# Performance work log

Measured on AMD Instinct MI355X. Metric: run time of the kernel, lower is better.

## Reference

```python
import jax, jax.numpy as jnp
import numpy as np

B, S, D, H = 4, 1024, 1024, 16
DH = D // H
NEG = -10000.0  # mask fill value for non-float32 (bool) masks in the torch code


def setup_inputs() -> dict:
    key = jax.random.key(0)
    ks = jax.random.split(key, 16)
    scale = 0.02
    inp = {
        "query": jax.random.normal(ks[0], (B, S, D), jnp.float32),
        "key": jax.random.normal(ks[1], (B, S, D), jnp.float32),
        "value": jax.random.normal(ks[2], (B, S, D), jnp.float32),
        "pos_embedding": jax.random.normal(ks[3], (B, S, D), jnp.float32),
        # learned params (torch Linear convention: y = x @ W.T + b, W is (out,in))
        "Wq": jax.random.normal(ks[4], (D, D), jnp.float32) * scale,
        "bq": jnp.zeros((D,), jnp.float32),
        "Wk": jax.random.normal(ks[5], (D, D), jnp.float32) * scale,
        "bk": jnp.zeros((D,), jnp.float32),
        "Wv": jax.random.normal(ks[6], (D, D), jnp.float32) * scale,
        "bv": jnp.zeros((D,), jnp.float32),
        "Wpos": jax.random.normal(ks[7], (D, D), jnp.float32) * scale,
        "u_bias": jax.random.normal(ks[8], (H, DH), jnp.float32) * scale,
        "v_bias": jax.random.normal(ks[9], (H, DH), jnp.float32) * scale,
        "Wout": jax.random.normal(ks[10], (D, D), jnp.float32) * scale,
        "bout": jnp.zeros((D,), jnp.float32),
    }
    # right-padding mask: lengths in [S//2, S]; mask[b,i,j] = pad(i) | pad(j)
    lengths = jax.random.randint(ks[11], (B,), S // 2, S + 1)
    pad = jnp.arange(S)[None, :] >= lengths[:, None]  # (B,S)
    inp["mask"] = pad[:, :, None] | pad[:, None, :]  # (B,S,S) bool
    return inp


def _relative_shift(pos_score, mask):
    """Batch-safe Transformer-XL relative shift (vectorized version of the
    per-batch python loop). pos_score: (B,H,S,S), mask: (B,S,S) bool."""
    b, h, s, _ = pos_score.shape
    # per-row true length: S - number of padded rows (column 0 is never padded)
    L = s - jnp.sum(mask[:, :, 0].astype(jnp.int32), axis=-1)  # (B,)
    i = jnp.arange(s)[:, None]
    j = jnp.arange(s)[None, :]

    def shift_one(ps, Lb):  # ps: (H,S,S), Lb: scalar int
        # padded[h,r,0]=0; padded[h,r,k]=ps[h,r,k-1]; flat index of out[i,j] in
        # the (Lb+1, Lb) reshape of padded[:, :Lb, :Lb+1], rows 1: -> offset Lb
        m = Lb + i * Lb + j            # (S,S)
        row = m // (Lb + 1)
        col = m % (Lb + 1)
        g = ps[:, jnp.clip(row, 0, s - 1), jnp.clip(col - 1, 0, s - 1)]  # (H,S,S)
        valid = (i < Lb) & (j < Lb) & (col != 0)
        return jnp.where(valid[None], g, jnp.zeros((), ps.dtype))

    shifted = jax.vmap(shift_one)(pos_score, L)
    # masked_fill_(padding_mask, 0.0)
    return jnp.where(mask[:, None, :, :], jnp.zeros((), pos_score.dtype), shifted)


def reference(query, key, value, pos_embedding, mask,
              Wq, bq, Wk, bk, Wv, bv, Wpos, u_bias, v_bias, Wout, bout):
    b = query.shape[0]
    sqrt_dim = np.sqrt(D).astype(np.float32)

    q = (query @ Wq.T + bq).reshape(b, -1, H, DH)                 # (B,S,H,dh)
    k = (key @ Wk.T + bk).reshape(b, -1, H, DH)                   # (B,S,H,dh)
    v = (value @ Wv.T + bv).reshape(b, -1, H, DH)                 # (B,S,H,dh)
    p = (pos_embedding @ Wpos.T).reshape(b, -1, H, DH)            # (B,S,H,dh)

    content_score = jnp.einsum('bqhd,bkhd->bhqk', q + u_bias, k)  # (B,H,S,S)
    pos_score = jnp.einsum('bqhd,bkhd->bhqk', q + v_bias, p)      # (B,H,S,S)
    pos_score = _relative_shift(pos_score, mask)

    score = (content_score + pos_score) / sqrt_dim
    m4 = mask[:, None, :, :]
    score = jnp.where(m4, NEG, score)
    attn = jax.nn.softmax(score, axis=-1)
    attn = jnp.where(m4, jnp.zeros((), attn.dtype), attn)
    # dropout is identity in eval mode
    context = jnp.einsum('bhqk,bkhd->bqhd', attn, v).reshape(b, -1, D)
    return context @ Wout.T + bout
```

## Files before the change

### kernel.cpp

```cpp
#include <hip/hip_runtime.h>

#define B_ 4
#define S_ 1024
#define D_ 1024
#define H_ 16
#define DH_ 64
#define OOS 0.03125f

#define QPL (1088 * 64)
#define KPL (1024 * 64)
#define VPL (1024 * 64)
#define PPL (200 * 1024)
#define PADLO 1056

#define APL_SW (256 * 32 * 512)
#define WPL_SW (64 * 32 * 512)

typedef __attribute__((ext_vector_type(8))) short short8;
typedef __attribute__((ext_vector_type(4))) float f32x4;
typedef const __attribute__((address_space(1))) unsigned int* gas_t;
typedef __attribute__((address_space(3))) unsigned int* las_t;

__device__ __forceinline__ ushort f2bf(float x) {
  unsigned u = __float_as_uint(x);
  unsigned r = u + 0x7fffu + ((u >> 16) & 1u);
  return (ushort)(r >> 16);
}
__device__ __forceinline__ float bf2f(ushort u) {
  return __uint_as_float(((unsigned)u) << 16);
}

union pack8 { ushort u[8]; uint4 v; };

struct ConvDesc { const float* src; ushort* hi; ushort* lo; };
struct ConvArgs { ConvDesc d[5]; };

__global__ __launch_bounds__(256) void conv_split(ConvArgs args)
{
  const ConvDesc dd = args.d[blockIdx.y];
  const int tt = blockIdx.x;
  const int tid = threadIdx.x;
  const float* src = dd.src + (size_t)tt * 16 * 1024;
  ushort* hi = dd.hi + (size_t)tt * 32 * 512;
  ushort* lo = dd.lo + (size_t)tt * 32 * 512;
#pragma unroll 4
  for (int q = 0; q < 16; ++q) {
    const int s = q * 256 + tid;
    const int r = s >> 8, c4 = s & 255;
    const float4 x = *(const float4*)(src + r * 1024 + c4 * 4);
    const int k = c4 * 4;
    const size_t addr = (size_t)(k >> 5) * 512 + ((k & 31) >> 3) * 128 + r * 8 + (k & 7);
    ushort4 hu, lu;
    hu.x = f2bf(x.x); lu.x = f2bf(x.x - bf2f(hu.x));
    hu.y = f2bf(x.y); lu.y = f2bf(x.y - bf2f(hu.y));
    hu.z = f2bf(x.z); lu.z = f2bf(x.z - bf2f(hu.z));
    hu.w = f2bf(x.w); lu.w = f2bf(x.w - bf2f(hu.w));
    *(ushort4*)(hi + addr) = hu;
    *(ushort4*)(lo + addr) = lu;
  }
}

template <int MODE>
__global__ __launch_bounds__(256, 2) void gemm_bf16x3(
    const ushort* __restrict__ Ahi, const ushort* __restrict__ Alo,
    const ushort* __restrict__ Bhi, const ushort* __restrict__ Blo,
    const float* __restrict__ bias, float* __restrict__ C,
    ushort* __restrict__ O1, ushort* __restrict__ O2,
    const float* __restrict__ ub, const float* __restrict__ vb)
{
  __shared__ __align__(16) ushort SM[12288];
  const int tid = threadIdx.x;
  const int wave = tid >> 6, lane = tid & 63;
  const int m16 = lane & 15, quad = lane >> 4;
  const int mw2 = wave & 1, nw2 = wave >> 1;
  const int mt0 = blockIdx.y * 4;
  const int nt0 = blockIdx.x * 8;

  f32x4 acc[2][4];
#pragma unroll
  for (int mf = 0; mf < 2; ++mf)
#pragma unroll
    for (int nf = 0; nf < 4; ++nf) acc[mf][nf] = (f32x4){0.f, 0.f, 0.f, 0.f};

  for (int kb = 0; kb < 32; ++kb) {
    __syncthreads();
    for (int t = wave; t < 24; t += 4) {
      const ushort* g;
      int l;
      if (t < 4)       { g = Ahi + ((size_t)(mt0 + t) * 32 + kb) * 512;      l = t * 512; }
      else if (t < 8)  { g = Alo + ((size_t)(mt0 + t - 4) * 32 + kb) * 512;  l = 2048 + (t - 4) * 512; }
      else if (t < 16) { g = Bhi + ((size_t)(nt0 + t - 8) * 32 + kb) * 512;  l = 4096 + (t - 8) * 512; }
      else             { g = Blo + ((size_t)(nt0 + t - 16) * 32 + kb) * 512; l = 8192 + (t - 16) * 512; }
      __builtin_amdgcn_global_load_lds((gas_t)(g + lane * 8), (las_t)(SM + l), 16, 0, 0);
    }
    __syncthreads();
    short8 ah[2], al[2], bh[4], bl[4];
#pragma unroll
    for (int mf = 0; mf < 2; ++mf) {
      ah[mf] = *(const short8*)(SM + (mw2 * 2 + mf) * 512 + lane * 8);
      al[mf] = *(const short8*)(SM + 2048 + (mw2 * 2 + mf) * 512 + lane * 8);
    }
#pragma unroll
    for (int nf = 0; nf < 4; ++nf) {
      bh[nf] = *(const short8*)(SM + 4096 + (nw2 * 4 + nf) * 512 + lane * 8);
      bl[nf] = *(const short8*)(SM + 8192 + (nw2 * 4 + nf) * 512 + lane * 8);
    }
#pragma unroll
    for (int mf = 0; mf < 2; ++mf)
#pragma unroll
      for (int nf = 0; nf < 4; ++nf) {
        acc[mf][nf] = __builtin_amdgcn_mfma_f32_16x16x32_bf16(ah[mf], bh[nf], acc[mf][nf], 0, 0, 0);
        acc[mf][nf] = __builtin_amdgcn_mfma_f32_16x16x32_bf16(ah[mf], bl[nf], acc[mf][nf], 0, 0, 0);
        acc[mf][nf] = __builtin_amdgcn_mfma_f32_16x16x32_bf16(al[mf], bh[nf], acc[mf][nf], 0, 0, 0);
      }
  }

  const int Mb = blockIdx.y * 64, Nb = blockIdx.x * 128;
  float* const E = (float*)SM;
#pragma unroll
  for (int c = 0; c < 2; ++c) {
    __syncthreads();
    if (nw2 == c) {
#pragma unroll
      for (int mf = 0; mf < 2; ++mf)
#pragma unroll
        for (int nf = 0; nf < 4; ++nf)
#pragma unroll
          for (int reg = 0; reg < 4; ++reg)
            E[(mw2 * 32 + mf * 16 + quad * 4 + reg) * 64 + nf * 16 + m16] = acc[mf][nf][reg];
    }
    __syncthreads();

    if (MODE == 3) {
#pragma unroll
      for (int q = 0; q < 2; ++q) {
        const int s = tid + 256 * q;
        const int cc = s & 63, rg = s >> 6;
        const int tok0 = Mb + rg * 8;
        const int n = Nb + c * 64 + cc;
        const int bb = tok0 >> 10, jr = tok0 & 1023;
        const int jt = jr >> 6, ksj = (jr >> 5) & 1, qk = (jr >> 3) & 3;
        const int h = n >> 6, dd = n & 63;
        const int subd = dd >> 4, nn = dd & 15;
        const size_t base = (size_t)(bb * 16 + h) * VPL + (size_t)jt * 4096 +
                            (size_t)(subd * 2 + ksj) * 512 + (qk * 16 + nn) * 8;
        const float bvv = bias[n];
        pack8 p;
#pragma unroll
        for (int i = 0; i < 8; ++i) p.u[i] = f2bf(E[(rg * 8 + i) * 64 + cc] + bvv);
        *(uint4*)(O1 + base) = p.v;
      }
    } else {
#pragma unroll
      for (int q = 0; q < 2; ++q) {
        const int s = tid + 256 * q;
        const int r = s >> 3, g = s & 7;
        const int token = Mb + r;
        const int n = Nb + c * 64 + g * 8;
        float v[8];
        *(float4*)&v[0] = *(const float4*)&E[r * 64 + g * 8];
        *(float4*)&v[4] = *(const float4*)&E[r * 64 + g * 8 + 4];
        if (MODE == 0) {
          float4 o0, o1;
          o0.x = v[0] + bias[n + 0]; o0.y = v[1] + bias[n + 1];
          o0.z = v[2] + bias[n + 2]; o0.w = v[3] + bias[n + 3];
          o1.x = v[4] + bias[n + 4]; o1.y = v[5] + bias[n + 5];
          o1.z = v[6] + bias[n + 6]; o1.w = v[7] + bias[n + 7];
          *(float4*)(C + (size_t)token * 1024 + n) = o0;
          *(float4*)(C + (size_t)token * 1024 + n + 4) = o1;
        } else if (MODE == 1) {
          const int bb = token >> 10, sr = token & 1023;
          const int h = n >> 6, d = n & 63;
          const size_t base = (size_t)(bb * 16 + h) * QPL + (size_t)sr * 64 + d;
          pack8 pu, pv;
#pragma unroll
          for (int j = 0; j < 8; ++j) {
            const float qv_ = v[j] + bias[n + j];
            pu.u[j] = f2bf(qv_ + ub[n + j]);
            pv.u[j] = f2bf(qv_ + vb[n + j]);
          }
          *(uint4*)(O1 + base) = pu.v;
          *(uint4*)(O2 + base) = pv.v;
        } else {
          const int bb = token >> 10, jr = token & 1023;
          const int h = n >> 6, dd = n & 63;
          const int ks = dd >> 5, qk = (dd >> 3) & 3;
          size_t base;
          if (MODE == 2)
            base = (size_t)(bb * 16 + h) * KPL + (size_t)(jr >> 6) * 4096 +
                   (size_t)((((jr >> 4) & 3) * 2 + ks)) * 512 + (qk * 16 + (jr & 15)) * 8;
          else {
            const int ro = jr + PADLO;
            base = (size_t)(bb * 16 + h) * PPL + (size_t)(ro >> 4) * 1024 +
                   (size_t)ks * 512 + (qk * 16 + (ro & 15)) * 8;
          }
          pack8 p;
#pragma unroll
          for (int j = 0; j < 8; ++j)
            p.u[j] = f2bf(v[j] + (MODE == 2 ? bias[n + j] : 0.f));
          *(uint4*)(O1 + base) = p.v;
        }
      }
    }
  }
}

__global__ void len_kernel(const int* __restrict__ mask, int* __restrict__ len,
                           ushort* __restrict__ Psw)
{
  const int b = blockIdx.x;
  int cnt = 0;
  for (int i = threadIdx.x; i < S_; i += 256)
    cnt += (mask[(size_t)b * S_ * S_ + (size_t)i * S_] != 0) ? 1 : 0;
  __shared__ int sh[256];
  sh[threadIdx.x] = cnt;
  __syncthreads();
  for (int off = 128; off > 0; off >>= 1) {
    if (threadIdx.x < off) sh[threadIdx.x] += sh[threadIdx.x + off];
    __syncthreads();
  }
  if (threadIdx.x == 0) len[b] = S_ - sh[0];
  for (int idx = threadIdx.x; idx < 16 * 64; idx += 256) {
    const int h = idx >> 6, d = idx & 63;
    Psw[(size_t)(b * 16 + h) * PPL + 65 * 1024 + (d >> 5) * 512 +
        (((d >> 3) & 3) * 16 + 15) * 8 + (d & 7)] = 0;
  }
}

__global__ __launch_bounds__(512, 4) void attn_mfma2(
    const ushort* __restrict__ Qu, const ushort* __restrict__ Qv,
    const ushort* __restrict__ Ksw, const ushort* __restrict__ Vsw,
    const ushort* __restrict__ Psw, const int* __restrict__ len,
    float* __restrict__ CTX)
{
  __shared__ __align__(16) ushort SMEM[26624];
  __shared__ float mrow[64], lrow[64], arow[64];

  ushort* const Ks_  = SMEM;
  ushort* const Vts_ = SMEM + 4096;
  ushort* const P1s_ = SMEM + 8192;
  ushort* const P2s_ = SMEM + 17408;
  float*  const sc   = (float*)(SMEM + 8192);
  ushort* const Pb   = SMEM + 17408;

  const int tid  = threadIdx.x;
  const int wave = tid >> 6, lane = tid & 63;
  const int hw   = wave >> 2, w4 = wave & 3;
  const int m16  = lane & 15, quad = lane >> 4;
  const int mw   = w4 & 1,  nw   = w4 >> 1;
  const int koff0 = quad * 8;

  const int base = blockIdx.x * 64;
  const int i0 = base + hw * 32;
  const int h  = blockIdx.y;
  const int b  = blockIdx.z;
  const int ph = b * 16 + h;
  const int L  = len[b];
  const size_t gb = ((size_t)b * S_) * D_ + h * DH_;

  if (base >= L) {
    for (int idx = tid; idx < 64 * 64; idx += 512) {
      const int r = idx >> 6, d = idx & 63;
      CTX[gb + (size_t)(base + r) * D_ + d] = 0.f;
    }
    return;
  }
  const bool active = (i0 < L);

  const ushort* quP = Qu + (size_t)ph * QPL;
  const ushort* qvP = Qv + (size_t)ph * QPL;
  short8 qufr[2][2], qvfr[2][2][2];
#pragma unroll
  for (int Mt = 0; Mt < 2; ++Mt)
#pragma unroll
    for (int ks = 0; ks < 2; ++ks) {
      qufr[Mt][ks] = *(const short8*)(quP + (size_t)(i0 + 16 * Mt + m16) * 64 + ks * 32 + koff0);
#pragma unroll
      for (int off = 0; off < 2; ++off)
        qvfr[off][Mt][ks] =
            *(const short8*)(qvP + (size_t)(i0 + off + 16 * Mt + m16) * 64 + ks * 32 + koff0);
    }

  if (tid < 64) { mrow[tid] = -3.0e38f; lrow[tid] = 0.f; arow[tid] = 0.f; }

  f32x4 ctx0 = {0.f, 0.f, 0.f, 0.f}, ctx1 = {0.f, 0.f, 0.f, 0.f};

  const ushort* ksP = Ksw + (size_t)ph * KPL;
  const ushort* vsP = Vsw + (size_t)ph * VPL;
  const ushort* psP = Psw + (size_t)ph * PPL;

  for (int j0 = 0; j0 < L; j0 += 64) {
    __syncthreads();

    const int jt = j0 >> 6;
    const int A1 = L - 32 - i0 + j0, A2 = j0 - i0 - 33;
    const int ro1 = A1 + PADLO, ro2 = A2 + PADLO;
    const int rb1 = ro1 >> 4, rb2 = ro2 >> 4;
    const int d1 = ro1 & 15, d2 = ro2 & 15;
    const int rb1lo = (L - 64 - base + j0 + PADLO) >> 4;
    const int rb2lo = (j0 - base - 65 + PADLO) >> 4;
    const ushort* P1h = P1s_ + ((rb1 - rb1lo) << 10);
    const ushort* P2h = P2s_ + ((rb2 - rb2lo) << 10);

    {
      const ushort* kgo = ksP + (size_t)jt * 4096;
      const ushort* vgo = vsP + (size_t)jt * 4096;
      const ushort* p1o = psP + (size_t)rb1lo * 1024;
      const ushort* p2o = psP + (size_t)rb2lo * 1024;
      for (int t = wave; t < 52; t += 8) {
        const ushort* g;
        int l;
        if (t < 8)       { g = kgo + t * 512;        l = t * 512; }
        else if (t < 16) { g = vgo + (t - 8) * 512;  l = 4096 + (t - 8) * 512; }
        else if (t < 34) { g = p1o + (t - 16) * 512; l = 8192 + (t - 16) * 512; }
        else             { g = p2o + (t - 34) * 512; l = 17408 + (t - 34) * 512; }
        __builtin_amdgcn_global_load_lds((gas_t)(g + lane * 8), (las_t)(SMEM + l), 16, 0, 0);
      }
    }
    __syncthreads();

    const int jrem = L - j0;
    const int jmax = (jrem < 64) ? jrem : 64;
    const int cthr = 31 + i0 - j0;

    f32x4 av[9];
#pragma unroll
    for (int t = 0; t < 9; ++t) {
      const int id = w4 + 4 * t;
      f32x4 a = {0.f, 0.f, 0.f, 0.f};
      if (active) {
        if (id < 8) {
          const int Mt = id & 1, Nt = id >> 1;
          if (16 * Nt < jmax) {
            const ushort* bp = Ks_ + (Nt * 2) * 512 + lane * 8;
            a = __builtin_amdgcn_mfma_f32_16x16x32_bf16(qufr[Mt][0], *(const short8*)bp, a, 0, 0, 0);
            a = __builtin_amdgcn_mfma_f32_16x16x32_bf16(qufr[Mt][1], *(const short8*)(bp + 512), a, 0, 0, 0);
          }
        } else if (id < 22) {
          const int e = id - 8, Mt = e & 1, Ntp = e >> 1;
          const int sm = 16 * (Ntp + Mt);
          if (sm >= d1 + 1 && sm <= jmax + d1 + 30 && 16 * Ntp - d1 <= cthr) {
            const ushort* bp = P1h + (Ntp * 2) * 512 + lane * 8;
            a = __builtin_amdgcn_mfma_f32_16x16x32_bf16(qvfr[0][Mt][0], *(const short8*)bp, a, 0, 0, 0);
            a = __builtin_amdgcn_mfma_f32_16x16x32_bf16(qvfr[0][Mt][1], *(const short8*)(bp + 512), a, 0, 0, 0);
          }
        } else {
          const int e = id - 22, Mt = e & 1, Ntp = e >> 1;
          const int sm = 16 * (Ntp + Mt);
          if (sm >= d2 + 1 && sm <= jmax + d2 + 30 && 16 * Ntp + 15 - d2 > cthr) {
            const ushort* bp = P2h + (Ntp * 2) * 512 + lane * 8;
            a = __builtin_amdgcn_mfma_f32_16x16x32_bf16(qvfr[1][Mt][0], *(const short8*)bp, a, 0, 0, 0);
            a = __builtin_amdgcn_mfma_f32_16x16x32_bf16(qvfr[1][Mt][1], *(const short8*)(bp + 512), a, 0, 0, 0);
          }
        }
      }
      av[t] = a;
    }
    __syncthreads();

#pragma unroll
    for (int t = 0; t < 2; ++t) {
      const int id = w4 + 4 * t;
      if (id < 8) {
        const int Mt = id & 1, Nt = id >> 1;
        if (16 * Nt < jmax) {
#pragma unroll
          for (int reg = 0; reg < 4; ++reg)
            sc[(hw * 32 + 16 * Mt + quad * 4 + reg) * 68 + 16 * Nt + m16] =
                active ? av[t][reg] : 0.f;
        }
      }
    }
    __syncthreads();

    if (active) {
#pragma unroll
      for (int t = 0; t < 9; ++t) {
        const int id = w4 + 4 * t;
        if (id >= 8) {
          const bool isG2 = id >= 22;
          const int e = id - (isG2 ? 22 : 8), Mt = e & 1, Ntp = e >> 1;
          const int dl = isG2 ? d2 : d1;
          const int sm = 16 * (Ntp + Mt);
          const bool use = sm >= dl + 1 && sm <= jmax + dl + 30 &&
                           (isG2 ? (16 * Ntp + 15 - dl > cthr) : (16 * Ntp - dl <= cthr));
          if (use) {
            const int c = 16 * Ntp + m16 - dl;
            const bool sel = isG2 ? (c > cthr) : (c <= cthr);
            if (sel) {
#pragma unroll
              for (int reg = 0; reg < 4; ++reg) {
                const int il = 16 * Mt + quad * 4 + reg;
                const int jl = c - 31 + il;
                if (jl >= 0 && jl < 64) sc[(hw * 32 + il) * 68 + jl] += av[t][reg];
              }
            }
          }
        }
      }
    }
    __syncthreads();

    {
      const int row = tid >> 3, t8 = tid & 7, jb = t8 * 8;
      const float* sr = sc + row * 68 + jb;
      float mx = -3.0e38f;
#pragma unroll
      for (int q = 0; q < 8; ++q)
        if (jb + q < jmax) mx = fmaxf(mx, sr[q]);
#pragma unroll
      for (int off = 1; off < 8; off <<= 1)
        mx = fmaxf(mx, __shfl_xor(mx, off, 64));
      if (t8 == 0) {
        const float mo = mrow[row];
        const float mn = fmaxf(mo, mx);
        arow[row] = __expf((mo - mn) * OOS);
        mrow[row] = mn;
      }
    }
    __syncthreads();
    {
      const int row = tid >> 3, t8 = tid & 7, jb = t8 * 8;
      const float m = mrow[row];
      const float* sr = sc + row * 68 + jb;
      float e[8], s = 0.f;
#pragma unroll
      for (int q = 0; q < 8; ++q) {
        float v = 0.f;
        if (jb + q < jmax) v = __expf((sr[q] - m) * OOS);
        e[q] = v;
        s += v;
      }
      ushort4 u0, u1;
      u0.x = f2bf(e[0]); u0.y = f2bf(e[1]); u0.z = f2bf(e[2]); u0.w = f2bf(e[3]);
      u1.x = f2bf(e[4]); u1.y = f2bf(e[5]); u1.z = f2bf(e[6]); u1.w = f2bf(e[7]);
      *(ushort4*)&Pb[row * 72 + jb] = u0;
      *(ushort4*)&Pb[row * 72 + jb + 4] = u1;
#pragma unroll
      for (int off = 1; off < 8; off <<= 1) s += __shfl_xor(s, off, 64);
      if (t8 == 0) lrow[row] = lrow[row] * arow[row] + s;
    }
    __syncthreads();

    if (active) {
      float al[4];
#pragma unroll
      for (int reg = 0; reg < 4; ++reg) al[reg] = arow[hw * 32 + 16 * mw + quad * 4 + reg];
#pragma unroll
      for (int reg = 0; reg < 4; ++reg) { ctx0[reg] *= al[reg]; ctx1[reg] *= al[reg]; }
      const ushort* ap = Pb + (hw * 32 + 16 * mw + m16) * 72;
#pragma unroll
      for (int ksj = 0; ksj < 2; ++ksj) {
        const short8 a = *(const short8*)(ap + ksj * 32 + koff0);
        ctx0 = __builtin_amdgcn_mfma_f32_16x16x32_bf16(
            a, *(const short8*)(Vts_ + ((nw * 2) * 2 + ksj) * 512 + lane * 8), ctx0, 0, 0, 0);
        ctx1 = __builtin_amdgcn_mfma_f32_16x16x32_bf16(
            a, *(const short8*)(Vts_ + ((nw * 2 + 1) * 2 + ksj) * 512 + lane * 8), ctx1, 0, 0, 0);
      }
    }
  }

#pragma unroll
  for (int reg = 0; reg < 4; ++reg) {
    const int il = 16 * mw + quad * 4 + reg;
    const int gi = i0 + il;
    const float inv = (active && gi < L) ? (1.f / lrow[hw * 32 + il]) : 0.f;
    CTX[gb + (size_t)gi * D_ + nw * 32 + m16]      = ctx0[reg] * inv;
    CTX[gb + (size_t)gi * D_ + nw * 32 + 16 + m16] = ctx1[reg] * inv;
  }
}

extern "C" void kernel_launch(void* const* d_in, const int* in_sizes, int n_in,
                              void* d_out, int out_size, void* d_ws, size_t ws_size,
                              hipStream_t stream)
{
  (void)in_sizes; (void)n_in; (void)out_size;
  const float* query = (const float*)d_in[0];
  const float* key   = (const float*)d_in[1];
  const float* value = (const float*)d_in[2];
  const float* pos   = (const float*)d_in[3];
  const float* Wq    = (const float*)d_in[4];
  const float* bq    = (const float*)d_in[5];
  const float* Wk    = (const float*)d_in[6];
  const float* bk    = (const float*)d_in[7];
  const float* Wv    = (const float*)d_in[8];
  const float* bv    = (const float*)d_in[9];
  const float* Wpos  = (const float*)d_in[10];
  const float* ub    = (const float*)d_in[11];
  const float* vb    = (const float*)d_in[12];
  const float* Wout  = (const float*)d_in[13];
  const float* bout  = (const float*)d_in[14];
  const int*   mask  = (const int*)d_in[15];

  char* cur = (char*)d_ws;
  auto take = [&](size_t bytes) {
    char* p = cur;
    cur += (bytes + 255) & ~(size_t)255;
    return p;
  };
  float*  CTX = (float*)take((size_t)4096 * 1024 * 4);
  ushort* Qu  = (ushort*)take((size_t)64 * QPL * 2);
  ushort* Qv  = (ushort*)take((size_t)64 * QPL * 2);
  ushort* Ksw = (ushort*)take((size_t)64 * KPL * 2);
  ushort* Vsw = (ushort*)take((size_t)64 * VPL * 2);
  ushort* Psw = (ushort*)take((size_t)64 * PPL * 2);
  ushort* Ah[4], *Al[4];
  for (int i = 0; i < 4; ++i) {
    Ah[i] = (ushort*)take((size_t)APL_SW * 2);
    Al[i] = (ushort*)take((size_t)APL_SW * 2);
  }
  ushort* Wh[5], *Wl[5];
  for (int i = 0; i < 5; ++i) {
    Wh[i] = (ushort*)take((size_t)WPL_SW * 2);
    Wl[i] = (ushort*)take((size_t)WPL_SW * 2);
  }
  int* len = (int*)take(256);
  ushort* Ch = Ah[0];
  ushort* Cl = Al[0];
  if (ws_size < (size_t)(cur - (char*)d_ws)) return;

  len_kernel<<<dim3(B_), dim3(256), 0, stream>>>(mask, len, Psw);

  {
    ConvArgs a;
    a.d[0] = {query, Ah[0], Al[0]};
    a.d[1] = {key,   Ah[1], Al[1]};
    a.d[2] = {value, Ah[2], Al[2]};
    a.d[3] = {pos,   Ah[3], Al[3]};
    a.d[4] = {query, Ah[0], Al[0]};
    conv_split<<<dim3(256, 4), dim3(256), 0, stream>>>(a);
    ConvArgs w;
    w.d[0] = {Wq,   Wh[0], Wl[0]};
    w.d[1] = {Wk,   Wh[1], Wl[1]};
    w.d[2] = {Wv,   Wh[2], Wl[2]};
    w.d[3] = {Wpos, Wh[3], Wl[3]};
    w.d[4] = {Wout, Wh[4], Wl[4]};
    conv_split<<<dim3(64, 5), dim3(256), 0, stream>>>(w);
  }

  const dim3 gblk(256), ggrid(1024 / 128, 4096 / 64);
  gemm_bf16x3<1><<<ggrid, gblk, 0, stream>>>(Ah[0], Al[0], Wh[0], Wl[0], bq, nullptr,
                                             Qu, Qv, ub, vb);
  gemm_bf16x3<2><<<ggrid, gblk, 0, stream>>>(Ah[1], Al[1], Wh[1], Wl[1], bk, nullptr,
                                             Ksw, nullptr, nullptr, nullptr);
  gemm_bf16x3<3><<<ggrid, gblk, 0, stream>>>(Ah[2], Al[2], Wh[2], Wl[2], bv, nullptr,
                                             Vsw, nullptr, nullptr, nullptr);
  gemm_bf16x3<4><<<ggrid, gblk, 0, stream>>>(Ah[3], Al[3], Wh[3], Wl[3], nullptr, nullptr,
                                             Psw, nullptr, nullptr, nullptr);

  attn_mfma2<<<dim3(S_ / 64, H_, B_), dim3(512), 0, stream>>>(
      Qu, Qv, Ksw, Vsw, Psw, len, CTX);

  {
    ConvArgs c;
    c.d[0] = {CTX, Ch, Cl};
    c.d[1] = c.d[0]; c.d[2] = c.d[0]; c.d[3] = c.d[0]; c.d[4] = c.d[0];
    conv_split<<<dim3(256, 1), dim3(256), 0, stream>>>(c);
  }

  gemm_bf16x3<0><<<ggrid, gblk, 0, stream>>>(Ch, Cl, Wh[4], Wl[4], bout, (float*)d_out,
                                             nullptr, nullptr, nullptr, nullptr);
}
```

Measured before the change: 734.3 us.

## Batch Q/K/V/P projections into one launch with 128x128 tiles

```diff
diff --git a/kernel.cpp b/kernel.cpp
--- a/kernel.cpp
+++ b/kernel.cpp
@@ -60,13 +60,159 @@
   }
 }
 
-template <int MODE>
-__global__ __launch_bounds__(256, 2) void gemm_bf16x3(
+struct GemmDesc {
+  const ushort* Ahi; const ushort* Alo;
+  const ushort* Bhi; const ushort* Blo;
+  const float* bias; ushort* O1; ushort* O2;
+  const float* ub; const float* vb; int mode; int pad;
+};
+struct GemmArgs { GemmDesc g[4]; };
+
+__global__ __launch_bounds__(256, 2) void gemm_fused(GemmArgs args)
+{
+  __shared__ __align__(16) ushort SM[16384];
+  const GemmDesc g = args.g[blockIdx.z];
+  const int tid = threadIdx.x;
+  const int wave = tid >> 6, lane = tid & 63;
+  const int m16 = lane & 15, quad = lane >> 4;
+  const int mw2 = wave & 1, nw2 = wave >> 1;
+  const int mt0 = blockIdx.y * 8;
+  const int nt0 = blockIdx.x * 8;
+
+  f32x4 acc[4][4];
+#pragma unroll
+  for (int mf = 0; mf < 4; ++mf)
+#pragma unroll
+    for (int nf = 0; nf < 4; ++nf) acc[mf][nf] = (f32x4){0.f, 0.f, 0.f, 0.f};
+
+  for (int kb = 0; kb < 32; ++kb) {
+    __syncthreads();
+    for (int t = wave; t < 32; t += 4) {
+      const ushort* gp;
+      int l;
+      if (t < 8)       { gp = g.Ahi + ((size_t)(mt0 + t) * 32 + kb) * 512;       l = t * 512; }
+      else if (t < 16) { gp = g.Alo + ((size_t)(mt0 + t - 8) * 32 + kb) * 512;   l = 4096 + (t - 8) * 512; }
+      else if (t < 24) { gp = g.Bhi + ((size_t)(nt0 + t - 16) * 32 + kb) * 512;  l = 8192 + (t - 16) * 512; }
+      else             { gp = g.Blo + ((size_t)(nt0 + t - 24) * 32 + kb) * 512;  l = 12288 + (t - 24) * 512; }
+      __builtin_amdgcn_global_load_lds((gas_t)(gp + lane * 8), (las_t)(SM + l), 16, 0, 0);
+    }
+    __syncthreads();
+    short8 ah[4], al[4], bh[4], bl[4];
+#pragma unroll
+    for (int mf = 0; mf < 4; ++mf) {
+      ah[mf] = *(const short8*)(SM + (mw2 * 4 + mf) * 512 + lane * 8);
+      al[mf] = *(const short8*)(SM + 4096 + (mw2 * 4 + mf) * 512 + lane * 8);
+    }
+#pragma unroll
+    for (int nf = 0; nf < 4; ++nf) {
+      bh[nf] = *(const short8*)(SM + 8192 + (nw2 * 4 + nf) * 512 + lane * 8);
+      bl[nf] = *(const short8*)(SM + 12288 + (nw2 * 4 + nf) * 512 + lane * 8);
+    }
+#pragma unroll
+    for (int mf = 0; mf < 4; ++mf)
+#pragma unroll
+      for (int nf = 0; nf < 4; ++nf) {
+        acc[mf][nf] = __builtin_amdgcn_mfma_f32_16x16x32_bf16(ah[mf], bh[nf], acc[mf][nf], 0, 0, 0);
+        acc[mf][nf] = __builtin_amdgcn_mfma_f32_16x16x32_bf16(ah[mf], bl[nf], acc[mf][nf], 0, 0, 0);
+        acc[mf][nf] = __builtin_amdgcn_mfma_f32_16x16x32_bf16(al[mf], bh[nf], acc[mf][nf], 0, 0, 0);
+      }
+  }
+
+  const int Mb = blockIdx.y * 128, Nb = blockIdx.x * 128;
+  float* const E0 = (float*)SM;
+  float* const E1 = (float*)(SM + 8192);
+#pragma unroll
+  for (int p = 0; p < 2; ++p) {
+    __syncthreads();
+    if (mw2 == p) {
+      float* const E = nw2 ? E1 : E0;
+#pragma unroll
+      for (int mf = 0; mf < 4; ++mf)
+#pragma unroll
+        for (int nf = 0; nf < 4; ++nf)
+#pragma unroll
+          for (int reg = 0; reg < 4; ++reg)
+            E[(mf * 16 + quad * 4 + reg) * 64 + nf * 16 + m16] = acc[mf][nf][reg];
+    }
+    __syncthreads();
+
+#pragma unroll
+    for (int cpart = 0; cpart < 2; ++cpart) {
+      float* const E = cpart ? E1 : E0;
+      const int tokBase = Mb + p * 64;
+      const int nBase = Nb + cpart * 64;
+
+      if (g.mode == 3) {
+#pragma unroll
+        for (int q = 0; q < 2; ++q) {
+          const int s = tid + 256 * q;
+          const int cc = s & 63, rg = s >> 6;
+          const int tok0 = tokBase + rg * 8;
+          const int n = nBase + cc;
+          const int bb = tok0 >> 10, jr = tok0 & 1023;
+          const int jt = jr >> 6, ksj = (jr >> 5) & 1, qk = (jr >> 3) & 3;
+          const int h = n >> 6, dd = n & 63;
+          const int subd = dd >> 4, nn = dd & 15;
+          const size_t base = (size_t)(bb * 16 + h) * VPL + (size_t)jt * 4096 +
+                              (size_t)(subd * 2 + ksj) * 512 + (qk * 16 + nn) * 8;
+          const float bvv = g.bias[n];
+          pack8 pk;
+#pragma unroll
+          for (int i = 0; i < 8; ++i) pk.u[i] = f2bf(E[(rg * 8 + i) * 64 + cc] + bvv);
+          *(uint4*)(g.O1 + base) = pk.v;
+        }
+      } else {
+#pragma unroll
+        for (int q = 0; q < 2; ++q) {
+          const int s = tid + 256 * q;
+          const int r = s >> 3, gc = s & 7;
+          const int token = tokBase + r;
+          const int n = nBase + gc * 8;
+          float v[8];
+          *(float4*)&v[0] = *(const float4*)&E[r * 64 + gc * 8];
+          *(float4*)&v[4] = *(const float4*)&E[r * 64 + gc * 8 + 4];
+          if (g.mode == 1) {
+            const int bb = token >> 10, sr = token & 1023;
+            const int h = n >> 6, d = n & 63;
+            const size_t base = (size_t)(bb * 16 + h) * QPL + (size_t)sr * 64 + d;
+            pack8 pu, pv;
+#pragma unroll
+            for (int j = 0; j < 8; ++j) {
+              const float qv_ = v[j] + g.bias[n + j];
+              pu.u[j] = f2bf(qv_ + g.ub[n + j]);
+              pv.u[j] = f2bf(qv_ + g.vb[n + j]);
+            }
+            *(uint4*)(g.O1 + base) = pu.v;
+            *(uint4*)(g.O2 + base) = pv.v;
+          } else {
+            const int bb = token >> 10, jr = token & 1023;
+            const int h = n >> 6, dd = n & 63;
+            const int ks = dd >> 5, qk = (dd >> 3) & 3;
+            size_t base;
+            if (g.mode == 2)
+              base = (size_t)(bb * 16 + h) * KPL + (size_t)(jr >> 6) * 4096 +
+                     (size_t)((((jr >> 4) & 3) * 2 + ks)) * 512 + (qk * 16 + (jr & 15)) * 8;
+            else {
+              const int ro = jr + PADLO;
+              base = (size_t)(bb * 16 + h) * PPL + (size_t)(ro >> 4) * 1024 +
+                     (size_t)ks * 512 + (qk * 16 + (ro & 15)) * 8;
+            }
+            pack8 pk;
+#pragma unroll
+            for (int j = 0; j < 8; ++j)
+              pk.u[j] = f2bf(v[j] + (g.mode == 2 ? g.bias[n + j] : 0.f));
+            *(uint4*)(g.O1 + base) = pk.v;
+          }
+        }
+      }
+    }
+  }
+}
+
+__global__ __launch_bounds__(256, 2) void gemm_out(
     const ushort* __restrict__ Ahi, const ushort* __restrict__ Alo,
     const ushort* __restrict__ Bhi, const ushort* __restrict__ Blo,
-    const float* __restrict__ bias, float* __restrict__ C,
-    ushort* __restrict__ O1, ushort* __restrict__ O2,
-    const float* __restrict__ ub, const float* __restrict__ vb)
+    const float* __restrict__ bias, float* __restrict__ C)
 {
   __shared__ __align__(16) ushort SM[12288];
   const int tid = threadIdx.x;
@@ -130,77 +276,22 @@
             E[(mw2 * 32 + mf * 16 + quad * 4 + reg) * 64 + nf * 16 + m16] = acc[mf][nf][reg];
     }
     __syncthreads();
-
-    if (MODE == 3) {
-#pragma unroll
-      for (int q = 0; q < 2; ++q) {
-        const int s = tid + 256 * q;
-        const int cc = s & 63, rg = s >> 6;
-        const int tok0 = Mb + rg * 8;
-        const int n = Nb + c * 64 + cc;
-        const int bb = tok0 >> 10, jr = tok0 & 1023;
-        const int jt = jr >> 6, ksj = (jr >> 5) & 1, qk = (jr >> 3) & 3;
-        const int h = n >> 6, dd = n & 63;
-        const int subd = dd >> 4, nn = dd & 15;
-        const size_t base = (size_t)(bb * 16 + h) * VPL + (size_t)jt * 4096 +
-                            (size_t)(subd * 2 + ksj) * 512 + (qk * 16 + nn) * 8;
-        const float bvv = bias[n];
-        pack8 p;
-#pragma unroll
-        for (int i = 0; i < 8; ++i) p.u[i] = f2bf(E[(rg * 8 + i) * 64 + cc] + bvv);
-        *(uint4*)(O1 + base) = p.v;
-      }
-    } else {
-#pragma unroll
-      for (int q = 0; q < 2; ++q) {
-        const int s = tid + 256 * q;
-        const int r = s >> 3, g = s & 7;
-        const int token = Mb + r;
-        const int n = Nb + c * 64 + g * 8;
-        float v[8];
-        *(float4*)&v[0] = *(const float4*)&E[r * 64 + g * 8];
-        *(float4*)&v[4] = *(const float4*)&E[r * 64 + g * 8 + 4];
-        if (MODE == 0) {
-          float4 o0, o1;
-          o0.x = v[0] + bias[n + 0]; o0.y = v[1] + bias[n + 1];
-          o0.z = v[2] + bias[n + 2]; o0.w = v[3] + bias[n + 3];
-          o1.x = v[4] + bias[n + 4]; o1.y = v[5] + bias[n + 5];
-          o1.z = v[6] + bias[n + 6]; o1.w = v[7] + bias[n + 7];
-          *(float4*)(C + (size_t)token * 1024 + n) = o0;
-          *(float4*)(C + (size_t)token * 1024 + n + 4) = o1;
-        } else if (MODE == 1) {
-          const int bb = token >> 10, sr = token & 1023;
-          const int h = n >> 6, d = n & 63;
-          const size_t base = (size_t)(bb * 16 + h) * QPL + (size_t)sr * 64 + d;
-          pack8 pu, pv;
-#pragma unroll
-          for (int j = 0; j < 8; ++j) {
-            const float qv_ = v[j] + bias[n + j];
-            pu.u[j] = f2bf(qv_ + ub[n + j]);
-            pv.u[j] = f2bf(qv_ + vb[n + j]);
-          }
-          *(uint4*)(O1 + base) = pu.v;
-          *(uint4*)(O2 + base) = pv.v;
-        } else {
-          const int bb = token >> 10, jr = token & 1023;
-          const int h = n >> 6, dd = n & 63;
-          const int ks = dd >> 5, qk = (dd >> 3) & 3;
-          size_t base;
-          if (MODE == 2)
-            base = (size_t)(bb * 16 + h) * KPL + (size_t)(jr >> 6) * 4096 +
-                   (size_t)((((jr >> 4) & 3) * 2 + ks)) * 512 + (qk * 16 + (jr & 15)) * 8;
-          else {
-            const int ro = jr + PADLO;
-            base = (size_t)(bb * 16 + h) * PPL + (size_t)(ro >> 4) * 1024 +
-                   (size_t)ks * 512 + (qk * 16 + (ro & 15)) * 8;
-          }
-          pack8 p;
-#pragma unroll
-          for (int j = 0; j < 8; ++j)
-            p.u[j] = f2bf(v[j] + (MODE == 2 ? bias[n + j] : 0.f));
-          *(uint4*)(O1 + base) = p.v;
-        }
-      }
+#pragma unroll
+    for (int q = 0; q < 2; ++q) {
+      const int s = tid + 256 * q;
+      const int r = s >> 3, g = s & 7;
+      const int token = Mb + r;
+      const int n = Nb + c * 64 + g * 8;
+      float v[8];
+      *(float4*)&v[0] = *(const float4*)&E[r * 64 + g * 8];
+      *(float4*)&v[4] = *(const float4*)&E[r * 64 + g * 8 + 4];
+      float4 o0, o1;
+      o0.x = v[0] + bias[n + 0]; o0.y = v[1] + bias[n + 1];
+      o0.z = v[2] + bias[n + 2]; o0.w = v[3] + bias[n + 3];
+      o1.x = v[4] + bias[n + 4]; o1.y = v[5] + bias[n + 5];
+      o1.z = v[6] + bias[n + 6]; o1.w = v[7] + bias[n + 7];
+      *(float4*)(C + (size_t)token * 1024 + n) = o0;
+      *(float4*)(C + (size_t)token * 1024 + n + 4) = o1;
     }
   }
 }
@@ -538,15 +629,14 @@
     conv_split<<<dim3(64, 5), dim3(256), 0, stream>>>(w);
   }
 
-  const dim3 gblk(256), ggrid(1024 / 128, 4096 / 64);
-  gemm_bf16x3<1><<<ggrid, gblk, 0, stream>>>(Ah[0], Al[0], Wh[0], Wl[0], bq, nullptr,
-                                             Qu, Qv, ub, vb);
-  gemm_bf16x3<2><<<ggrid, gblk, 0, stream>>>(Ah[1], Al[1], Wh[1], Wl[1], bk, nullptr,
-                                             Ksw, nullptr, nullptr, nullptr);
-  gemm_bf16x3<3><<<ggrid, gblk, 0, stream>>>(Ah[2], Al[2], Wh[2], Wl[2], bv, nullptr,
-                                             Vsw, nullptr, nullptr, nullptr);
-  gemm_bf16x3<4><<<ggrid, gblk, 0, stream>>>(Ah[3], Al[3], Wh[3], Wl[3], nullptr, nullptr,
-                                             Psw, nullptr, nullptr, nullptr);
+  {
+    GemmArgs ga;
+    ga.g[0] = {Ah[0], Al[0], Wh[0], Wl[0], bq, Qu, Qv, ub, vb, 1, 0};
+    ga.g[1] = {Ah[1], Al[1], Wh[1], Wl[1], bk, Ksw, nullptr, nullptr, nullptr, 2, 0};
+    ga.g[2] = {Ah[2], Al[2], Wh[2], Wl[2], bv, Vsw, nullptr, nullptr, nullptr, 3, 0};
+    ga.g[3] = {Ah[3], Al[3], Wh[3], Wl[3], nullptr, Psw, nullptr, nullptr, nullptr, 4, 0};
+    gemm_fused<<<dim3(8, 32, 4), dim3(256), 0, stream>>>(ga);
+  }
 
   attn_mfma2<<<dim3(S_ / 64, H_, B_), dim3(512), 0, stream>>>(
       Qu, Qv, Ksw, Vsw, Psw, len, CTX);
@@ -558,6 +648,6 @@
     conv_split<<<dim3(256, 1), dim3(256), 0, stream>>>(c);
   }
 
-  gemm_bf16x3<0><<<ggrid, gblk, 0, stream>>>(Ch, Cl, Wh[4], Wl[4], bout, (float*)d_out,
-                                             nullptr, nullptr, nullptr, nullptr);
-}
+  gemm_out<<<dim3(8, 64), dim3(256), 0, stream>>>(Ch, Cl, Wh[4], Wl[4], bout,
+                                                  (float*)d_out);
+}
```

Result: faster. 675.1 us (-8.1%).
